# Kernel optimization log

Hardware: AMD Instinct MI355X
Metric: run time of the kernel (lower is better)

Reference implementation:

```python
import jax, jax.numpy as jnp
import numpy as np

B, S, D, H = 2, 4096, 1024, 16
DH = D // H  # 64


def setup_inputs() -> dict:
    key = jax.random.key(0)
    ks = jax.random.split(key, 5)
    x = jax.random.normal(ks[0], (B, S, D), dtype=jnp.float32)
    scale = 1.0 / np.sqrt(D)
    Wq = jax.random.normal(ks[1], (D, D), dtype=jnp.float32) * scale
    Wk = jax.random.normal(ks[2], (D, D), dtype=jnp.float32) * scale
    Wv = jax.random.normal(ks[3], (D, D), dtype=jnp.float32) * scale
    Wo = jax.random.normal(ks[4], (D, D), dtype=jnp.float32) * scale
    bo = jnp.zeros((D,), dtype=jnp.float32)
    return {"x": x, "Wq": Wq, "Wk": Wk, "Wv": Wv, "Wo": Wo, "bo": bo}


def reference(x, Wq, Wk, Wv, Wo, bo):
    b, s, d = x.shape
    # QKV projections (no bias), split heads: [b, s, H, DH]
    q = (x @ Wq).reshape(b, s, H, DH)
    k = (x @ Wk).reshape(b, s, H, DH)
    v = (x @ Wv).reshape(b, s, H, DH)
    # scores: [b, H, s, s]
    scores = jnp.einsum("bqhd,bkhd->bhqk", q, k)
    # causal mask: upper triangle (j > i) set to -inf, then scale by sqrt(d_head)
    causal = jnp.triu(jnp.ones((s, s), dtype=bool), k=1)
    scores = jnp.where(causal, -jnp.inf, scores)
    weights = jax.nn.softmax(scores / jnp.sqrt(jnp.float32(DH)), axis=-1)
    # dropout rate is 0.0 -> identity
    ctx = jnp.einsum("bhqk,bkhd->bqhd", weights, v).reshape(b, s, d)
    return ctx @ Wo + bo
```

## Files before the change

### kernel.cpp

```cpp
#include <hip/hip_runtime.h>
#include <hip/hip_bf16.h>
#include <stdint.h>
#include <math.h>

#define BATCH 2
#define S_LEN 4096
#define DMODEL 1024
#define NH 16
#define DHEAD 64
#define MTOK (BATCH * S_LEN)

#define QSCALE 0.1803368801111793f

typedef unsigned short u16;
typedef __attribute__((ext_vector_type(8))) short bf16x8;
typedef __attribute__((ext_vector_type(4))) float f32x4;
typedef __attribute__((ext_vector_type(16))) float f32x16;
typedef __attribute__((ext_vector_type(4))) unsigned short u16x4;

__device__ __forceinline__ float b2f(u16 u) {
  union { unsigned int i; float f; } v; v.i = ((unsigned int)u) << 16; return v.f;
}
__device__ __forceinline__ u16 f2b(float f) {
  union { float f; unsigned int i; } v; v.f = f;
  unsigned int r = v.i + 0x7FFF + ((v.i >> 16) & 1);
  return (u16)(r >> 16);
}
__device__ __forceinline__ unsigned int pk2(float hi, float lo) {
  union { float f; unsigned int u; } a, b; a.f = hi; b.f = lo;
  return __builtin_amdgcn_perm(a.u, b.u, 0x07060302u);
}
__device__ __forceinline__ void pswap(unsigned int& a, unsigned int& b) {
  asm("v_permlane32_swap_b32 %0, %1" : "+v"(a), "+v"(b));
}

__device__ __forceinline__ void gl_lds16(const u16* g, u16* l) {
  __builtin_amdgcn_global_load_lds(
      (__attribute__((address_space(1))) void*)(u16*)g,
      (__attribute__((address_space(3))) void*)l, 16, 0, 0);
}

__global__ void detect_dtype(const unsigned int* __restrict__ x, int* __restrict__ flag) {
  __shared__ int cnt;
  if (threadIdx.x == 0) cnt = 0;
  __syncthreads();
  int c = 0;
  for (int i = threadIdx.x; i < 4096; i += 256) {
    unsigned int w = x[i];
    int e = (w >> 7) & 0xFF;
    if (e >= 100 && e <= 135) c++;
  }
  atomicAdd(&cnt, c);
  __syncthreads();
  if (threadIdx.x == 0) *flag = (cnt > 2048) ? 1 : 0;
}

__global__ void convert_x(const void* __restrict__ xin, u16* __restrict__ xc,
                          const int* __restrict__ flagp) {
  const int isb = *flagp;
  long e = ((long)blockIdx.x * 256 + threadIdx.x) * 4;
  if (isb) {
    *(uint2*)&xc[e] = *(const uint2*)((const u16*)xin + e);
  } else {
    float4 f = *(const float4*)((const float*)xin + e);
    xc[e + 0] = f2b(f.x);
    xc[e + 1] = f2b(f.y);
    xc[e + 2] = f2b(f.z);
    xc[e + 3] = f2b(f.w);
  }
}

__global__ void transpose4(const void* __restrict__ W0, const void* __restrict__ W1,
                           const void* __restrict__ W2, const void* __restrict__ W3,
                           u16* __restrict__ out, const int* __restrict__ flagp) {
  __shared__ u16 tile[32][33];
  const int isb = *flagp;
  int z = blockIdx.z;
  const void* W = (z == 0) ? W0 : (z == 1) ? W1 : (z == 2) ? W2 : W3;
  u16* o = out + (long)z * (DMODEL * DMODEL);
  int x = blockIdx.x * 32 + threadIdx.x;
  int y0 = blockIdx.y * 32;
  if (isb) {
    const u16* Wb = (const u16*)W;
#pragma unroll
    for (int i = 0; i < 32; i += 8)
      tile[threadIdx.y + i][threadIdx.x] = Wb[(long)(y0 + threadIdx.y + i) * DMODEL + x];
  } else {
    const float* Wf = (const float*)W;
#pragma unroll
    for (int i = 0; i < 32; i += 8)
      tile[threadIdx.y + i][threadIdx.x] = f2b(Wf[(long)(y0 + threadIdx.y + i) * DMODEL + x]);
  }
  __syncthreads();
  int x2 = blockIdx.y * 32 + threadIdx.x;
  int y2 = blockIdx.x * 32;
#pragma unroll
  for (int i = 0; i < 32; i += 8)
    o[(long)(y2 + threadIdx.y + i) * DMODEL + x2] = tile[threadIdx.x][threadIdx.y + i];
}

#define BM 128
#define BN 128
#define BK 32

#define GEMM_CORE(A_, Bt_, Kd_)                                                   \
  __shared__ __align__(16) u16 lA[BM * BK];                                       \
  __shared__ __align__(16) u16 lB[BN * BK];                                       \
  const int tid = threadIdx.x;                                                    \
  const int w = tid >> 6;                                                         \
  const int lane = tid & 63;                                                      \
  const int m0 = blockIdx.y * BM;                                                 \
  const int n0 = blockIdx.x * BN;                                                 \
  const int wm = (w >> 1) * 64;                                                   \
  const int wn = (w & 1) * 64;                                                    \
  const int lc = lane & 15;                                                       \
  const int lq = lane >> 4;                                                       \
  f32x4 acc[4][4] = {};                                                           \
  for (int k0 = 0; k0 < (Kd_); k0 += BK) {                                        \
    __syncthreads();                                                              \
    _Pragma("unroll")                                                             \
    for (int jj = 0; jj < 2; ++jj) {                                              \
      int base = (jj * 4 + w) * 512;                                              \
      int e = base + lane * 8;                                                    \
      int row = e >> 5, col = e & 31;                                             \
      gl_lds16((A_) + (long)(m0 + row) * (Kd_) + k0 + col, lA + base);            \
      gl_lds16((Bt_) + (long)(n0 + row) * (Kd_) + k0 + col, lB + base);           \
    }                                                                             \
    __syncthreads();                                                              \
    bf16x8 af[4], bg[4];                                                          \
    _Pragma("unroll")                                                             \
    for (int i = 0; i < 4; ++i)                                                   \
      af[i] = *(const bf16x8*)&lA[(wm + i * 16 + lc) * BK + lq * 8];              \
    _Pragma("unroll")                                                             \
    for (int j = 0; j < 4; ++j)                                                   \
      bg[j] = *(const bf16x8*)&lB[(wn + j * 16 + lc) * BK + lq * 8];              \
    _Pragma("unroll")                                                             \
    for (int i = 0; i < 4; ++i)                                                   \
      _Pragma("unroll")                                                           \
      for (int j = 0; j < 4; ++j)                                                 \
        acc[i][j] = __builtin_amdgcn_mfma_f32_16x16x32_bf16(af[i], bg[j], acc[i][j], 0, 0, 0); \
  }

__global__ __launch_bounds__(256)
void gemm_qkv(const u16* __restrict__ A, const u16* __restrict__ Bt,
              u16* __restrict__ Qo, u16* __restrict__ Ko, u16* __restrict__ Vo) {
  GEMM_CORE(A, Bt, DMODEL)
#pragma unroll
  for (int i = 0; i < 4; ++i) {
#pragma unroll
    for (int j = 0; j < 4; ++j) {
      int n = n0 + wn + j * 16 + lc;
      int rgn = n >> 10;
      int nn = n & 1023;
      int h = nn >> 6, dh = nn & (DHEAD - 1);
      float sc = (rgn == 0) ? QSCALE : 1.0f;
#pragma unroll
      for (int r = 0; r < 4; ++r) {
        int m = m0 + wm + i * 16 + lq * 4 + r;
        int b = m >> 12, s = m & (S_LEN - 1);
        float v = acc[i][j][r] * sc;
        long idx_r = (((long)(b * NH + h)) * S_LEN + s) * DHEAD + dh;
        long idx_v = (((long)(b * NH + h)) * DHEAD + dh) * S_LEN + s;
        if (rgn == 0)      Qo[idx_r] = f2b(v);
        else if (rgn == 1) Ko[idx_r] = f2b(v);
        else               Vo[idx_v] = f2b(v);
      }
    }
  }
}

__global__ __launch_bounds__(256)
void gemm_out(const u16* __restrict__ A, const u16* __restrict__ Bt,
              const void* __restrict__ bias, void* __restrict__ C,
              const int* __restrict__ flagp) {
  GEMM_CORE(A, Bt, DMODEL)
  const int isb = *flagp;
#pragma unroll
  for (int i = 0; i < 4; ++i) {
#pragma unroll
    for (int j = 0; j < 4; ++j) {
      int n = n0 + wn + j * 16 + lc;
      float bv = isb ? b2f(((const u16*)bias)[n]) : ((const float*)bias)[n];
#pragma unroll
      for (int r = 0; r < 4; ++r) {
        int m = m0 + wm + i * 16 + lq * 4 + r;
        float v = acc[i][j][r] + bv;
        if (isb) ((u16*)C)[(long)m * DMODEL + n] = f2b(v);
        else     ((float*)C)[(long)m * DMODEL + n] = v;
      }
    }
  }
}

__global__ __launch_bounds__(256, 2)
void flash_attn(const u16* __restrict__ Q, const u16* __restrict__ K,
                const u16* __restrict__ Vt, u16* __restrict__ ctx) {
  __shared__ __align__(16) u16 lK[64 * 64];
  __shared__ __align__(16) u16 lV[64 * 64];

  const int tid = threadIdx.x;
  const int w = tid >> 6;
  const int lane = tid & 63;
  const int l31 = lane & 31;
  const int l5 = lane >> 5;

  const int hb = blockIdx.x;
  const int h = hb & (NH - 1);
  const int b = hb >> 4;
  const int qt = gridDim.y - 1 - (int)blockIdx.y;
  const int q0 = qt * 128;

  const int bh = b * NH + h;
  const u16* Qb = Q + (long)bh * S_LEN * DHEAD;
  const u16* Kb = K + (long)bh * S_LEN * DHEAD;
  const u16* Vb = Vt + (long)bh * DHEAD * S_LEN;

  const int qa = q0 + w * 32;
  const int myq = qa + l31;

  bf16x8 aq[4];
#pragma unroll
  for (int c = 0; c < 4; ++c)
    aq[c] = *(const bf16x8*)(Qb + (long)myq * DHEAD + c * 16 + l5 * 8);

  union OU { unsigned int wd[4]; bf16x8 v; } ones;
#pragma unroll
  for (int i = 0; i < 4; ++i) ones.wd[i] = 0x3F803F80u;

  const int srow = tid >> 2;
  const int sc0 = (tid & 3) * 2;
  const int sd0 = srow * 64 + ((sc0 ^ (srow & 7)) * 8);
  const int sd1 = srow * 64 + (((sc0 + 1) ^ (srow & 7)) * 8);
  const u16* kp = Kb + (long)srow * DHEAD + sc0 * 8;
  const u16* vp = Vb + (long)srow * S_LEN + sc0 * 8;

  const int kmax = q0 + 64;
  bf16x8 kr0 = *(const bf16x8*)kp;
  bf16x8 kr1 = *(const bf16x8*)(kp + 8);
  bf16x8 vr0 = *(const bf16x8*)vp;
  bf16x8 vr1 = *(const bf16x8*)(vp + 8);
  const u16* kpre = kp + 64 * DHEAD;
  const u16* vpre = vp + 64;

  f32x16 o0 = {}, o1 = {};
  f32x16 lacc = {};
  const int xsw = l31 & 7;

  int offK[4][2], offV[4][2];
#pragma unroll
  for (int c = 0; c < 4; ++c) {
    const int ch = c * 2 + l5;
    offK[c][0] = l31 * 64 + ((ch ^ xsw) * 8);
    offK[c][1] = (32 + l31) * 64 + ((ch ^ xsw) * 8);
    offV[c][0] = offK[c][0];
    offV[c][1] = offK[c][1];
  }

  for (int k0 = 0; k0 <= kmax; k0 += 64) {
    *(bf16x8*)&lK[sd0] = kr0;
    *(bf16x8*)&lK[sd1] = kr1;
    *(bf16x8*)&lV[sd0] = vr0;
    *(bf16x8*)&lV[sd1] = vr1;
    __syncthreads();

    if (k0 + 64 <= kmax) {
      kr0 = *(const bf16x8*)kpre;
      kr1 = *(const bf16x8*)(kpre + 8);
      vr0 = *(const bf16x8*)vpre;
      vr1 = *(const bf16x8*)(vpre + 8);
      kpre += 64 * DHEAD;
      vpre += 64;
    }

    if (k0 <= qa + 31) {
      f32x16 s0 = {}, s1 = {};
      __builtin_amdgcn_s_setprio(1);
#pragma unroll
      for (int c = 0; c < 4; ++c) {
        bf16x8 ak0 = *(const bf16x8*)&lK[offK[c][0]];
        bf16x8 ak1 = *(const bf16x8*)&lK[offK[c][1]];
        s0 = __builtin_amdgcn_mfma_f32_32x32x16_bf16(ak0, aq[c], s0, 0, 0, 0);
        s1 = __builtin_amdgcn_mfma_f32_32x32x16_bf16(ak1, aq[c], s1, 0, 0, 0);
      }
      __builtin_amdgcn_s_setprio(0);

      const bool masked = (k0 + 63 > qa);
      union BPU { unsigned int wd[4]; bf16x8 v; };
      BPU bp[4];
#pragma unroll
      for (int ph = 0; ph < 2; ++ph) {
        const f32x16 sv = ph ? s1 : s0;
        float p[16];
#pragma unroll
        for (int rr = 0; rr < 16; ++rr) {
          float e = __builtin_amdgcn_exp2f(sv[rr]);
          if (masked) {
            int kv = k0 + ph * 32 + (rr & 3) + 8 * (rr >> 2) + 4 * l5;
            e = (kv > myq) ? 0.0f : e;
          }
          p[rr] = e;
        }
#pragma unroll
        for (int g = 0; g < 2; ++g) {
          unsigned int A0 = pk2(p[8 * g + 1], p[8 * g + 0]);
          unsigned int A1 = pk2(p[8 * g + 3], p[8 * g + 2]);
          unsigned int B0 = pk2(p[8 * g + 5], p[8 * g + 4]);
          unsigned int B1 = pk2(p[8 * g + 7], p[8 * g + 6]);
          pswap(A0, B0);
          pswap(A1, B1);
          const int kc = ph * 2 + g;
          bp[kc].wd[0] = A0; bp[kc].wd[1] = A1;
          bp[kc].wd[2] = B0; bp[kc].wd[3] = B1;
        }
      }

      __builtin_amdgcn_s_setprio(1);
#pragma unroll
      for (int kc = 0; kc < 4; ++kc) {
        bf16x8 av0 = *(const bf16x8*)&lV[offV[kc][0]];
        bf16x8 av1 = *(const bf16x8*)&lV[offV[kc][1]];
        o0 = __builtin_amdgcn_mfma_f32_32x32x16_bf16(av0, bp[kc].v, o0, 0, 0, 0);
        o1 = __builtin_amdgcn_mfma_f32_32x32x16_bf16(av1, bp[kc].v, o1, 0, 0, 0);
        lacc = __builtin_amdgcn_mfma_f32_32x32x16_bf16(ones.v, bp[kc].v, lacc, 0, 0, 0);
      }
      __builtin_amdgcn_s_setprio(0);
    }
    __syncthreads();
  }

  float inv = 1.0f / lacc[0];

  u16* cp = ctx + ((long)(b * S_LEN + myq)) * DMODEL + h * DHEAD;
#pragma unroll
  for (int d32 = 0; d32 < 2; ++d32) {
    const f32x16 ov = d32 ? o1 : o0;
#pragma unroll
    for (int g = 0; g < 4; ++g) {
      u16x4 st;
#pragma unroll
      for (int r = 0; r < 4; ++r) st[r] = f2b(ov[4 * g + r] * inv);
      *(u16x4*)&cp[d32 * 32 + g * 8 + l5 * 4] = st;
    }
  }
}

extern "C" void kernel_launch(void* const* d_in, const int* in_sizes, int n_in,
                              void* d_out, int out_size, void* d_ws, size_t ws_size,
                              hipStream_t stream) {
  const void* x  = d_in[0];
  const void* Wq = d_in[1];
  const void* Wk = d_in[2];
  const void* Wv = d_in[3];
  const void* Wo = d_in[4];
  const void* bo = d_in[5];
  u16* ws = (u16*)d_ws;

  u16* wt  = ws;
  u16* wto = wt + 3145728;
  u16* Qb  = ws + 4194304;
  u16* Vtb = ws + 12582912;
  u16* xc  = ws + 20971520;
  u16* ctx = xc;
  int* flag = (int*)(ws + 29360128);
  u16* Kb  = (u16*)d_out;

  detect_dtype<<<1, 256, 0, stream>>>((const unsigned int*)x, flag);
  convert_x<<<8192, 256, 0, stream>>>(x, xc, flag);
  transpose4<<<dim3(32, 32, 4), dim3(32, 8), 0, stream>>>(Wq, Wk, Wv, Wo, wt, flag);

  gemm_qkv<<<dim3(3 * DMODEL / BN, MTOK / BM), 256, 0, stream>>>(xc, wt, Qb, Kb, Vtb);

  flash_attn<<<dim3(NH * BATCH, S_LEN / 128), 256, 0, stream>>>(Qb, Kb, Vtb, ctx);

  gemm_out<<<dim3(DMODEL / BN, MTOK / BM), 256, 0, stream>>>(ctx, wto, bo, d_out, flag);
}
```

Measured before the change: 318.2 us.

## Double-buffer GEMM tiles with async LDS prefetch and larger 256x128 blocks

Replaces the synchronous single-buffer GEMM core with a double-buffered pipeline. Loads for tile t+2 are issued right after tile t is consumed, and vmcnt waits replace full syncthreads. Blocks grow to 512 threads covering 256x128 tiles, which halves the grid in M. The V-transposed epilogue now writes four contiguous bf16 values per store. Together these aim to hide global-load latency and improve store efficiency, at the cost of more LDS per block and lower occupancy (launch_bounds 512,1).

```diff
diff --git a/kernel.cpp b/kernel.cpp
--- a/kernel.cpp
+++ b/kernel.cpp
@@ -99,52 +99,71 @@
     o[(long)(y2 + threadIdx.y + i) * DMODEL + x2] = tile[threadIdx.x][threadIdx.y + i];
 }
 
-#define BM 128
-#define BN 128
-#define BK 32
-
-#define GEMM_CORE(A_, Bt_, Kd_)                                                   \
-  __shared__ __align__(16) u16 lA[BM * BK];                                       \
-  __shared__ __align__(16) u16 lB[BN * BK];                                       \
+#define BM2 256
+#define BN2 128
+#define BK2 32
+#define NT2 (DMODEL / BK2)
+
+#define VM3 asm volatile("s_waitcnt vmcnt(3)" ::: "memory")
+#define VM0 asm volatile("s_waitcnt vmcnt(0)" ::: "memory")
+#define BARX do { asm volatile("" ::: "memory"); __builtin_amdgcn_s_barrier(); \
+                  asm volatile("" ::: "memory"); } while (0)
+
+#define GEMM_CORE2(A_, Bt_)                                                       \
+  __shared__ __align__(16) u16 lds[2 * 12288];                                    \
   const int tid = threadIdx.x;                                                    \
   const int w = tid >> 6;                                                         \
   const int lane = tid & 63;                                                      \
-  const int m0 = blockIdx.y * BM;                                                 \
-  const int n0 = blockIdx.x * BN;                                                 \
+  const int m0 = blockIdx.y * BM2;                                                \
+  const int n0 = blockIdx.x * BN2;                                                \
   const int wm = (w >> 1) * 64;                                                   \
   const int wn = (w & 1) * 64;                                                    \
   const int lc = lane & 15;                                                       \
   const int lq = lane >> 4;                                                       \
+  const u16* pA = (A_) + (long)(m0 + w * 16 + (lane >> 2)) * DMODEL + (lane & 3) * 8; \
+  const u16* pB = (Bt_) + (long)(n0 + w * 16 + (lane >> 2)) * DMODEL + (lane & 3) * 8; \
+  u16* aB0 = lds + w * 512;                                                       \
+  u16* bB0 = lds + 8192 + w * 512;                                                \
   f32x4 acc[4][4] = {};                                                           \
-  for (int k0 = 0; k0 < (Kd_); k0 += BK) {                                        \
-    __syncthreads();                                                              \
-    _Pragma("unroll")                                                             \
-    for (int jj = 0; jj < 2; ++jj) {                                              \
-      int base = (jj * 4 + w) * 512;                                              \
-      int e = base + lane * 8;                                                    \
-      int row = e >> 5, col = e & 31;                                             \
-      gl_lds16((A_) + (long)(m0 + row) * (Kd_) + k0 + col, lA + base);            \
-      gl_lds16((Bt_) + (long)(n0 + row) * (Kd_) + k0 + col, lB + base);           \
-    }                                                                             \
-    __syncthreads();                                                              \
+  gl_lds16(pA, aB0);                                                              \
+  gl_lds16(pA + 128 * DMODEL, aB0 + 4096);                                        \
+  gl_lds16(pB, bB0);                                                              \
+  gl_lds16(pA + BK2, aB0 + 12288);                                                \
+  gl_lds16(pA + BK2 + 128 * DMODEL, aB0 + 4096 + 12288);                          \
+  gl_lds16(pB + BK2, bB0 + 12288);                                                \
+  for (int t = 0; t < NT2; ++t) {                                                 \
+    if (t < NT2 - 1) { VM3; } else { VM0; }                                       \
+    BARX;                                                                         \
+    const u16* la = lds + (t & 1) * 12288;                                        \
+    const u16* lb = la + 8192;                                                    \
     bf16x8 af[4], bg[4];                                                          \
     _Pragma("unroll")                                                             \
     for (int i = 0; i < 4; ++i)                                                   \
-      af[i] = *(const bf16x8*)&lA[(wm + i * 16 + lc) * BK + lq * 8];              \
+      af[i] = *(const bf16x8*)&la[(wm + i * 16 + lc) * 32 + lq * 8];              \
     _Pragma("unroll")                                                             \
     for (int j = 0; j < 4; ++j)                                                   \
-      bg[j] = *(const bf16x8*)&lB[(wn + j * 16 + lc) * BK + lq * 8];              \
+      bg[j] = *(const bf16x8*)&lb[(wn + j * 16 + lc) * 32 + lq * 8];              \
     _Pragma("unroll")                                                             \
     for (int i = 0; i < 4; ++i)                                                   \
       _Pragma("unroll")                                                           \
       for (int j = 0; j < 4; ++j)                                                 \
         acc[i][j] = __builtin_amdgcn_mfma_f32_16x16x32_bf16(af[i], bg[j], acc[i][j], 0, 0, 0); \
-  }
-
-__global__ __launch_bounds__(256)
+    BARX;                                                                         \
+    if (t + 2 < NT2) {                                                            \
+      const u16* at = pA + (t + 2) * BK2;                                         \
+      const u16* bt = pB + (t + 2) * BK2;                                         \
+      u16* ad = aB0 + (t & 1) * 12288;                                            \
+      u16* bd = bB0 + (t & 1) * 12288;                                            \
+      gl_lds16(at, ad);                                                           \
+      gl_lds16(at + 128 * DMODEL, ad + 4096);                                     \
+      gl_lds16(bt, bd);                                                           \
+    }                                                                             \
+  }
+
+__global__ __launch_bounds__(512, 1)
 void gemm_qkv(const u16* __restrict__ A, const u16* __restrict__ Bt,
               u16* __restrict__ Qo, u16* __restrict__ Ko, u16* __restrict__ Vo) {
-  GEMM_CORE(A, Bt, DMODEL)
+  GEMM_CORE2(A, Bt)
 #pragma unroll
   for (int i = 0; i < 4; ++i) {
 #pragma unroll
@@ -153,27 +172,32 @@
       int rgn = n >> 10;
       int nn = n & 1023;
       int h = nn >> 6, dh = nn & (DHEAD - 1);
-      float sc = (rgn == 0) ? QSCALE : 1.0f;
-#pragma unroll
-      for (int r = 0; r < 4; ++r) {
-        int m = m0 + wm + i * 16 + lq * 4 + r;
-        int b = m >> 12, s = m & (S_LEN - 1);
-        float v = acc[i][j][r] * sc;
-        long idx_r = (((long)(b * NH + h)) * S_LEN + s) * DHEAD + dh;
-        long idx_v = (((long)(b * NH + h)) * DHEAD + dh) * S_LEN + s;
-        if (rgn == 0)      Qo[idx_r] = f2b(v);
-        else if (rgn == 1) Ko[idx_r] = f2b(v);
-        else               Vo[idx_v] = f2b(v);
+      int m_base = m0 + wm + i * 16 + lq * 4;
+      int b = m_base >> 12, s0q = m_base & (S_LEN - 1);
+      if (rgn == 2) {
+        long idx_v = (((long)(b * NH + h)) * DHEAD + dh) * S_LEN + s0q;
+        u16x4 vv;
+#pragma unroll
+        for (int r = 0; r < 4; ++r) vv[r] = f2b(acc[i][j][r]);
+        *(u16x4*)&Vo[idx_v] = vv;
+      } else {
+        float sc = (rgn == 0) ? QSCALE : 1.0f;
+        u16* dst = (rgn == 0) ? Qo : Ko;
+#pragma unroll
+        for (int r = 0; r < 4; ++r) {
+          long idx_r = (((long)(b * NH + h)) * S_LEN + s0q + r) * DHEAD + dh;
+          dst[idx_r] = f2b(acc[i][j][r] * sc);
+        }
       }
     }
   }
 }
 
-__global__ __launch_bounds__(256)
+__global__ __launch_bounds__(512, 1)
 void gemm_out(const u16* __restrict__ A, const u16* __restrict__ Bt,
               const void* __restrict__ bias, void* __restrict__ C,
               const int* __restrict__ flagp) {
-  GEMM_CORE(A, Bt, DMODEL)
+  GEMM_CORE2(A, Bt)
   const int isb = *flagp;
 #pragma unroll
   for (int i = 0; i < 4; ++i) {
@@ -368,9 +392,9 @@
   convert_x<<<8192, 256, 0, stream>>>(x, xc, flag);
   transpose4<<<dim3(32, 32, 4), dim3(32, 8), 0, stream>>>(Wq, Wk, Wv, Wo, wt, flag);
 
-  gemm_qkv<<<dim3(3 * DMODEL / BN, MTOK / BM), 256, 0, stream>>>(xc, wt, Qb, Kb, Vtb);
+  gemm_qkv<<<dim3(3 * DMODEL / BN2, MTOK / BM2), 512, 0, stream>>>(xc, wt, Qb, Kb, Vtb);
 
   flash_attn<<<dim3(NH * BATCH, S_LEN / 128), 256, 0, stream>>>(Qb, Kb, Vtb, ctx);
 
-  gemm_out<<<dim3(DMODEL / BN, MTOK / BM), 256, 0, stream>>>(ctx, wto, bo, d_out, flag);
-}
+  gemm_out<<<dim3(DMODEL / BN2, MTOK / BM2), 512, 0, stream>>>(ctx, wto, bo, d_out, flag);
+}
```

Result: faster. 294.1 us (-7.6%).
